# Performance work log

Measured on AMD Instinct MI355X. Metric: run time of the kernel, lower is better.

The kernel has to match this reference:

```python
import jax, jax.numpy as jnp
import numpy as np
import math

B, T, D, H = 4, 2048, 1024, 16
HD = D // H  # 64

def setup_inputs() -> dict:
    key = jax.random.key(0)
    ks = jax.random.split(key, 11)
    s = 1.0 / math.sqrt(D)
    return {
        "q": jax.random.normal(ks[0], (B, T, D), jnp.float32),
        "k": jax.random.normal(ks[1], (B, T, D), jnp.float32),
        "v": jax.random.normal(ks[2], (B, T, D), jnp.float32),
        "Wq": jax.random.normal(ks[3], (D, D), jnp.float32) * s,
        "bq": jnp.zeros((D,), jnp.float32),
        "Wk": jax.random.normal(ks[4], (D, D), jnp.float32) * s,
        "bk": jnp.zeros((D,), jnp.float32),
        "Wv": jax.random.normal(ks[5], (D, D), jnp.float32) * s,
        "bv": jnp.zeros((D,), jnp.float32),
        "Wo": jax.random.normal(ks[6], (D, D), jnp.float32) * s,
        "bo": jnp.zeros((D,), jnp.float32),
    }

def reference(q, k, v, Wq, bq, Wk, bk, Wv, bv, Wo, bo):
    # Linear projections (torch Linear: x @ W.T + b)
    qp = q @ Wq.T + bq
    kp = k @ Wk.T + bk
    vp = v @ Wv.T + bv
    # [B, T, D] -> [B, H, T, HD]
    def split(x):
        return x.reshape(B, T, H, HD).transpose(0, 2, 1, 3)
    qh, kh, vh = split(qp), split(kp), split(vp)
    # scaled dot-product attention
    score = jnp.einsum('bhqd,bhkd->bhqk', qh, kh) / math.sqrt(HD)
    attn = jax.nn.softmax(score, axis=-1)
    out = jnp.einsum('bhqk,bhkd->bhqd', attn, vh)
    # merge heads and output projection
    out = out.transpose(0, 2, 1, 3).reshape(B, T, D)
    return out @ Wo.T + bo
```

## Files before the change

kernel.cpp:

```cpp
#include <hip/hip_runtime.h>
#include <hip/hip_bf16.h>
#include <stdint.h>

#define B_ 4
#define T_ 2048
#define D_ 1024
#define H_ 16
#define HD_ 64
#define NKT (T_ / 64)

typedef __bf16 bf16;
typedef __bf16 bf16x8 __attribute__((ext_vector_type(8)));
typedef __bf16 bf16x4 __attribute__((ext_vector_type(4)));
typedef float f32x4 __attribute__((ext_vector_type(4)));
typedef uint32_t u32x4 __attribute__((ext_vector_type(4)));

#define QSCALE 0.18033688011112042f

__device__ __forceinline__ float fast_exp2(float x) {
#if __has_builtin(__builtin_amdgcn_exp2f)
    return __builtin_amdgcn_exp2f(x);
#else
    return exp2f(x);
#endif
}

__device__ __forceinline__ void async_load16(const bf16* g, const bf16* lds_uniform) {
    __builtin_amdgcn_global_load_lds(
        (const __attribute__((address_space(1))) uint32_t*)(uintptr_t)g,
        (__attribute__((address_space(3))) uint32_t*)(uintptr_t)lds_uniform,
        16, 0, 0);
}

__device__ __forceinline__ uint32_t pack2_bf16(float lo, float hi) {
    union { uint32_t u; __bf16 h[2]; } r;
    r.h[0] = (__bf16)lo;
    r.h[1] = (__bf16)hi;
    return r.u;
}

__device__ __forceinline__ void permswap16(uint32_t& a, uint32_t& b) {
    asm("v_permlane16_swap_b32 %0, %1" : "+v"(a), "+v"(b));
}

__global__ __launch_bounds__(256) void cast3(const float* __restrict__ s0, bf16* __restrict__ d0,
                                             const float* __restrict__ s1, bf16* __restrict__ d1,
                                             const float* __restrict__ s2, bf16* __restrict__ d2,
                                             int n4) {
    const float* s = blockIdx.y == 0 ? s0 : (blockIdx.y == 1 ? s1 : s2);
    bf16* d = blockIdx.y == 0 ? d0 : (blockIdx.y == 1 ? d1 : d2);
    int i = blockIdx.x * 256 + threadIdx.x;
    if (i < n4) {
        f32x4 v = ((const f32x4*)s)[i];
        bf16x4 o;
        o.x = (bf16)v.x; o.y = (bf16)v.y; o.z = (bf16)v.z; o.w = (bf16)v.w;
        ((bf16x4*)d)[i] = o;
    }
}

__global__ __launch_bounds__(256) void cast4(const float* __restrict__ s0, bf16* __restrict__ d0,
                                             const float* __restrict__ s1, bf16* __restrict__ d1,
                                             const float* __restrict__ s2, bf16* __restrict__ d2,
                                             const float* __restrict__ s3, bf16* __restrict__ d3,
                                             int n4) {
    const float* s = blockIdx.y == 0 ? s0 : (blockIdx.y == 1 ? s1 : (blockIdx.y == 2 ? s2 : s3));
    bf16* d = blockIdx.y == 0 ? d0 : (blockIdx.y == 1 ? d1 : (blockIdx.y == 2 ? d2 : d3));
    int i = blockIdx.x * 256 + threadIdx.x;
    if (i < n4) {
        f32x4 v = ((const f32x4*)s)[i];
        bf16x4 o;
        o.x = (bf16)v.x; o.y = (bf16)v.y; o.z = (bf16)v.z; o.w = (bf16)v.w;
        ((bf16x4*)d)[i] = o;
    }
}

template <typename OutT, int VMODE>
__device__ __forceinline__ void gemm_body(const bf16* __restrict__ A,
                                          const bf16* __restrict__ W,
                                          const float* __restrict__ bias,
                                          OutT* __restrict__ C,
                                          int lin, float scale,
                                          bf16* As, bf16* Bs, bf16* Tt) {
    const int K = D_, N = D_;
    const int tid = threadIdx.x;
    const int wid = tid >> 6, lane = tid & 63;
    const int quad = lane >> 4, l15 = lane & 15;
    const int wm = (wid >> 1) * 64, wn = (wid & 1) * 64;
    const int bx = N >> 7;
    const int ty = (lin & 7) + 8 * (lin / (8 * bx));
    const int tx = (lin >> 3) % bx;
    const long rowA0 = (long)ty * 128;
    const long rowB0 = (long)tx * 128;
    const int srow = lane >> 2;
    const int schunk = (lane & 3) * 8;
    const int sbase = (wid * 32) * 32;

    f32x4 acc[4][4];
#pragma unroll
    for (int i = 0; i < 4; i++)
#pragma unroll
        for (int j = 0; j < 4; j++) acc[i][j] = (f32x4){0.f, 0.f, 0.f, 0.f};

#pragma unroll
    for (int s = 0; s < 2; s++) {
        int r = wid * 32 + s * 16 + srow;
        async_load16(&A[(rowA0 + r) * K + schunk], &As[sbase + s * 16 * 32]);
        async_load16(&W[(rowB0 + r) * K + schunk], &Bs[sbase + s * 16 * 32]);
    }
    __syncthreads();

    const int NIT = K >> 5;
    for (int it = 0; it < NIT; it++) {
        const int cur = it & 1;
        const int co = cur * (128 * 32);
        if (it + 1 < NIT) {
            const int k1 = (it + 1) << 5;
            const int no = (cur ^ 1) * (128 * 32);
#pragma unroll
            for (int s = 0; s < 2; s++) {
                int r = wid * 32 + s * 16 + srow;
                async_load16(&A[(rowA0 + r) * K + k1 + schunk], &As[no + sbase + s * 16 * 32]);
                async_load16(&W[(rowB0 + r) * K + k1 + schunk], &Bs[no + sbase + s * 16 * 32]);
            }
        }
        bf16x8 af[4], bfr[4];
#pragma unroll
        for (int i = 0; i < 4; i++)
            af[i] = *(const bf16x8*)&As[co + (wm + i * 16 + l15) * 32 + quad * 8];
#pragma unroll
        for (int j = 0; j < 4; j++)
            bfr[j] = *(const bf16x8*)&Bs[co + (wn + j * 16 + l15) * 32 + quad * 8];
#pragma unroll
        for (int i = 0; i < 4; i++)
#pragma unroll
            for (int j = 0; j < 4; j++)
                acc[i][j] = __builtin_amdgcn_mfma_f32_16x16x32_bf16(af[i], bfr[j],
                                                                    acc[i][j], 0, 0, 0);
        __syncthreads();
    }

    if constexpr (VMODE == 0) {
#pragma unroll
        for (int i = 0; i < 4; i++) {
            long m = rowA0 + wm + i * 16 + quad * 4;
#pragma unroll
            for (int j = 0; j < 4; j++) {
                long n = rowB0 + wn + j * 16 + l15;
                float bb = bias[n];
#pragma unroll
                for (int r = 0; r < 4; r++) {
                    float v = (acc[i][j][r] + bb) * scale;
                    C[(m + r) * N + n] = (OutT)v;
                }
            }
        }
    } else {
#pragma unroll
        for (int i = 0; i < 4; i++) {
            int ml = wm + i * 16 + quad * 4;
#pragma unroll
            for (int j = 0; j < 4; j++) {
                int nl = wn + j * 16 + l15;
                float bb = bias[rowB0 + nl];
                bf16x4 ov = {(bf16)(acc[i][j][0] + bb), (bf16)(acc[i][j][1] + bb),
                             (bf16)(acc[i][j][2] + bb), (bf16)(acc[i][j][3] + bb)};
                *(bf16x4*)&Tt[nl * 136 + ml] = ov;
            }
        }
        __syncthreads();
        const long bidx = rowA0 >> 11;
        const int t0 = (int)(rowA0 & 2047);
#pragma unroll
        for (int p = 0; p < 8; p++) {
            int nl = p * 16 + (tid >> 4);
            int c = tid & 15;
            bf16x8 val = *(const bf16x8*)&Tt[nl * 136 + c * 8];
            int n = (int)rowB0 + nl;
            long vrow = (bidx * H_ + (n >> 6)) * (long)HD_ + (n & 63);
            int cp = (c & ~3) | ((c & 1) << 1) | ((c & 2) >> 1);
            *(bf16x8*)&((bf16*)C)[vrow * T_ + t0 + cp * 8] = val;
        }
    }
}

__global__ __launch_bounds__(256) void gemm_qkv(const bf16* __restrict__ Xq,
                                                const bf16* __restrict__ WqB,
                                                const float* __restrict__ bq,
                                                bf16* __restrict__ Qp,
                                                const bf16* __restrict__ Xk,
                                                const bf16* __restrict__ WkB,
                                                const float* __restrict__ bk,
                                                bf16* __restrict__ Kp,
                                                const bf16* __restrict__ Xv,
                                                const bf16* __restrict__ WvB,
                                                const float* __restrict__ bv,
                                                bf16* __restrict__ VtG) {
    __shared__ __align__(16) char sm[34816];
    bf16* As = (bf16*)sm;
    bf16* Bs = (bf16*)(sm + 16384);
    bf16* Tt = (bf16*)sm;
    const int p = blockIdx.x >> 9;
    const int lin = blockIdx.x & 511;
    if (p == 0)
        gemm_body<bf16, 0>(Xq, WqB, bq, Qp, lin, QSCALE, As, Bs, Tt);
    else if (p == 1)
        gemm_body<bf16, 0>(Xk, WkB, bk, Kp, lin, 1.f, As, Bs, Tt);
    else
        gemm_body<bf16, 1>(Xv, WvB, bv, VtG, lin, 1.f, As, Bs, Tt);
}

__global__ __launch_bounds__(256) void gemm_out(const bf16* __restrict__ Op,
                                                const bf16* __restrict__ WoB,
                                                const float* __restrict__ bo,
                                                float* __restrict__ out) {
    __shared__ __align__(16) char sm[32768];
    bf16* As = (bf16*)sm;
    bf16* Bs = (bf16*)(sm + 16384);
    gemm_body<float, 0>(Op, WoB, bo, out, blockIdx.x, 1.f, As, Bs, nullptr);
}

__global__ __launch_bounds__(256, 4) void attn_kernel(const bf16* __restrict__ Qp,
                                                      const bf16* __restrict__ Kp,
                                                      const bf16* __restrict__ VT,
                                                      bf16* __restrict__ Op) {
    __shared__ bf16 smem[4][64 * 64];
    const int tid = threadIdx.x;
    const int wid = tid >> 6, lane = tid & 63;
    const int quad = lane >> 4, l15 = lane & 15;
    const int q7 = l15 & 7;
    const int lin = blockIdx.x;
    const int bh = (lin & 7) + 8 * (lin >> 7);
    const int qt = (lin >> 3) & 15;
    const int b = bh >> 4, h = bh & 15;
    const long tok0 = (long)b * T_ + (long)qt * 128 + wid * 32;
    const int hcol = h * HD_;
    const long vrow0 = ((long)bh) * HD_;
    const int g_sw = ((lane & 7) ^ (lane >> 3)) * 8;
    const int srow = lane >> 3;
    const int sbase = (wid * 16) * 64;

    {
        const long krow0 = (long)b * T_;
#pragma unroll
        for (int s = 0; s < 2; s++) {
            int r = wid * 16 + s * 8 + srow;
            async_load16(&Kp[(krow0 + r) * D_ + hcol + g_sw], &smem[0][sbase + s * 8 * 64]);
            async_load16(&VT[(vrow0 + r) * T_ + g_sw], &smem[2][sbase + s * 8 * 64]);
        }
    }

    bf16x8 bq[2][2];
#pragma unroll
    for (int nt = 0; nt < 2; nt++)
#pragma unroll
        for (int ks = 0; ks < 2; ks++)
            bq[nt][ks] = *(const bf16x8*)&Qp[(tok0 + nt * 16 + l15) * D_ + hcol +
                                             ks * 32 + quad * 8];

    f32x4 o[4][2];
#pragma unroll
    for (int mt = 0; mt < 4; mt++)
#pragma unroll
        for (int nt = 0; nt < 2; nt++) o[mt][nt] = (f32x4){0.f, 0.f, 0.f, 0.f};
    float lsum[2] = {0.f, 0.f};

    __syncthreads();

    for (int kt = 0; kt < NKT; kt++) {
        const int cur = kt & 1;
        if (kt + 1 < NKT) {
            const long krow1 = (long)b * T_ + (long)(kt + 1) * 64;
            const int nb = cur ^ 1;
#pragma unroll
            for (int s = 0; s < 2; s++) {
                int r = wid * 16 + s * 8 + srow;
                async_load16(&Kp[(krow1 + r) * D_ + hcol + g_sw], &smem[nb][sbase + s * 8 * 64]);
                async_load16(&VT[(vrow0 + r) * T_ + (long)(kt + 1) * 64 + g_sw],
                             &smem[2 + nb][sbase + s * 8 * 64]);
            }
        }
        const bf16* Ksc = smem[cur];
        const bf16* Vsc = smem[2 + cur];

        bf16x8 pb0[2];
        {
            uint32_t pA[2][2], pB[2][2];
#pragma unroll
            for (int mt = 0; mt < 2; mt++) {
                bf16x8 ak0 = *(const bf16x8*)&Ksc[(mt * 16 + l15) * 64 + ((quad ^ q7) * 8)];
                bf16x8 ak1 = *(const bf16x8*)&Ksc[(mt * 16 + l15) * 64 + (((4 + quad) ^ q7) * 8)];
#pragma unroll
                for (int nt = 0; nt < 2; nt++) {
                    f32x4 s = {0.f, 0.f, 0.f, 0.f};
                    s = __builtin_amdgcn_mfma_f32_16x16x32_bf16(ak0, bq[nt][0], s, 0, 0, 0);
                    s = __builtin_amdgcn_mfma_f32_16x16x32_bf16(ak1, bq[nt][1], s, 0, 0, 0);
                    float p0 = fast_exp2(s[0]), p1 = fast_exp2(s[1]);
                    float p2 = fast_exp2(s[2]), p3 = fast_exp2(s[3]);
                    lsum[nt] += (p0 + p1) + (p2 + p3);
                    pA[mt][nt] = pack2_bf16(p0, p1);
                    pB[mt][nt] = pack2_bf16(p2, p3);
                }
            }
#pragma unroll
            for (int nt = 0; nt < 2; nt++) {
                permswap16(pA[0][nt], pA[1][nt]);
                permswap16(pB[0][nt], pB[1][nt]);
                u32x4 f = {pA[0][nt], pB[0][nt], pA[1][nt], pB[1][nt]};
                pb0[nt] = __builtin_bit_cast(bf16x8, f);
            }
        }
#pragma unroll
        for (int mt = 0; mt < 4; mt++) {
            bf16x8 av0 = *(const bf16x8*)&Vsc[(mt * 16 + l15) * 64 + ((quad ^ q7) * 8)];
#pragma unroll
            for (int nt = 0; nt < 2; nt++)
                o[mt][nt] = __builtin_amdgcn_mfma_f32_16x16x32_bf16(av0, pb0[nt],
                                                                    o[mt][nt], 0, 0, 0);
        }
        bf16x8 pb1[2];
        {
            uint32_t pA[2][2], pB[2][2];
#pragma unroll
            for (int mt = 0; mt < 2; mt++) {
                bf16x8 ak0 = *(const bf16x8*)&Ksc[((2 + mt) * 16 + l15) * 64 + ((quad ^ q7) * 8)];
                bf16x8 ak1 = *(const bf16x8*)&Ksc[((2 + mt) * 16 + l15) * 64 +
                                                  (((4 + quad) ^ q7) * 8)];
#pragma unroll
                for (int nt = 0; nt < 2; nt++) {
                    f32x4 s = {0.f, 0.f, 0.f, 0.f};
                    s = __builtin_amdgcn_mfma_f32_16x16x32_bf16(ak0, bq[nt][0], s, 0, 0, 0);
                    s = __builtin_amdgcn_mfma_f32_16x16x32_bf16(ak1, bq[nt][1], s, 0, 0, 0);
                    float p0 = fast_exp2(s[0]), p1 = fast_exp2(s[1]);
                    float p2 = fast_exp2(s[2]), p3 = fast_exp2(s[3]);
                    lsum[nt] += (p0 + p1) + (p2 + p3);
                    pA[mt][nt] = pack2_bf16(p0, p1);
                    pB[mt][nt] = pack2_bf16(p2, p3);
                }
            }
#pragma unroll
            for (int nt = 0; nt < 2; nt++) {
                permswap16(pA[0][nt], pA[1][nt]);
                permswap16(pB[0][nt], pB[1][nt]);
                u32x4 f = {pA[0][nt], pB[0][nt], pA[1][nt], pB[1][nt]};
                pb1[nt] = __builtin_bit_cast(bf16x8, f);
            }
        }
#pragma unroll
        for (int mt = 0; mt < 4; mt++) {
            bf16x8 av1 = *(const bf16x8*)&Vsc[(mt * 16 + l15) * 64 + (((4 + quad) ^ q7) * 8)];
#pragma unroll
            for (int nt = 0; nt < 2; nt++)
                o[mt][nt] = __builtin_amdgcn_mfma_f32_16x16x32_bf16(av1, pb1[nt],
                                                                    o[mt][nt], 0, 0, 0);
        }
        __syncthreads();
    }

#pragma unroll
    for (int nt = 0; nt < 2; nt++) {
        lsum[nt] += __shfl_xor(lsum[nt], 16, 64);
        lsum[nt] += __shfl_xor(lsum[nt], 32, 64);
        lsum[nt] = 1.f / lsum[nt];
    }

    bf16* ew = &smem[wid][0];
#pragma unroll
    for (int mt = 0; mt < 4; mt++)
#pragma unroll
        for (int nt = 0; nt < 2; nt++) {
            bf16x4 ov = {(bf16)(o[mt][nt][0] * lsum[nt]), (bf16)(o[mt][nt][1] * lsum[nt]),
                         (bf16)(o[mt][nt][2] * lsum[nt]), (bf16)(o[mt][nt][3] * lsum[nt])};
            *(bf16x4*)&ew[(nt * 16 + l15) * 64 +
                          (((mt * 2 + (quad >> 1)) ^ q7) * 8) + (quad & 1) * 4] = ov;
        }
#pragma unroll
    for (int p2 = 0; p2 < 4; p2++) {
        int q = p2 * 8 + (lane >> 3);
        int dc = lane & 7;
        bf16x8 ov = *(const bf16x8*)&ew[q * 64 + ((dc ^ (q & 7)) * 8)];
        *(bf16x8*)&Op[(tok0 + q) * D_ + hcol + dc * 8] = ov;
    }
}

extern "C" void kernel_launch(void* const* d_in, const int* in_sizes, int n_in,
                              void* d_out, int out_size, void* d_ws, size_t ws_size,
                              hipStream_t stream) {
    const float* q  = (const float*)d_in[0];
    const float* k  = (const float*)d_in[1];
    const float* v  = (const float*)d_in[2];
    const float* Wq = (const float*)d_in[3];
    const float* bq = (const float*)d_in[4];
    const float* Wk = (const float*)d_in[5];
    const float* bk = (const float*)d_in[6];
    const float* Wv = (const float*)d_in[7];
    const float* bv = (const float*)d_in[8];
    const float* Wo = (const float*)d_in[9];
    const float* bo = (const float*)d_in[10];
    float* out = (float*)d_out;

    const size_t MD = (size_t)B_ * T_ * D_;
    const size_t DD = (size_t)D_ * D_;
    char* ws = (char*)d_ws;
    bf16* Xq  = (bf16*)ws; ws += MD * 2;
    bf16* Xk  = (bf16*)ws; ws += MD * 2;
    bf16* Xv  = (bf16*)ws; ws += MD * 2;
    bf16* WqB = (bf16*)ws; ws += DD * 2;
    bf16* WkB = (bf16*)ws; ws += DD * 2;
    bf16* WvB = (bf16*)ws; ws += DD * 2;
    bf16* WoB = (bf16*)ws; ws += DD * 2;
    bf16* Qp  = (bf16*)ws; ws += MD * 2;
    bf16* Kp  = (bf16*)ws; ws += MD * 2;
    bf16* VtG = (bf16*)ws; ws += MD * 2;
    bf16* Op  = (bf16*)ws; ws += MD * 2;

    cast3<<<dim3(MD / 4 / 256, 3), 256, 0, stream>>>(q, Xq, k, Xk, v, Xv, MD / 4);
    cast4<<<dim3(DD / 4 / 256, 4), 256, 0, stream>>>(Wq, WqB, Wk, WkB, Wv, WvB, Wo, WoB, DD / 4);

    gemm_qkv<<<3 * 512, 256, 0, stream>>>(Xq, WqB, bq, Qp, Xk, WkB, bk, Kp, Xv, WvB, bv, VtG);

    attn_kernel<<<B_ * H_ * (T_ / 128), 256, 0, stream>>>(Qp, Kp, VtG, Op);

    gemm_out<<<512, 256, 0, stream>>>(Op, WoB, bo, out);
}
```

Measured before the change: 331.8 us.

## Use 8 waves per attention block with 16 query rows each, MFMA row sums

The attention kernel moves from 4 waves handling 32 query rows each to 8 waves handling 16 query rows each. Each wave now loads one row per K/V tile. This cuts per-wave register use and raises wave count for latency hiding. The softmax denominator is now computed with an MFMA against a ones vector instead of scalar adds and shuffles, and s_setprio brackets the PV MFMAs. In exchange, each K/V tile in shared memory is reused by fewer query rows per wave, and the MFMA count per block rises because of the extra row-sum MFMAs.

Measured after the change: 339.1 us. +2.2%, slower.

```diff
diff --git a/kernel.cpp b/kernel.cpp
--- a/kernel.cpp
+++ b/kernel.cpp
@@ -219,7 +219,7 @@
     gemm_body<float, 0>(Op, WoB, bo, out, blockIdx.x, 1.f, As, Bs, nullptr);
 }
 
-__global__ __launch_bounds__(256, 4) void attn_kernel(const bf16* __restrict__ Qp,
+__global__ __launch_bounds__(512, 8) void attn_kernel(const bf16* __restrict__ Qp,
                                                       const bf16* __restrict__ Kp,
                                                       const bf16* __restrict__ VT,
                                                       bf16* __restrict__ Op) {
@@ -232,37 +232,30 @@
     const int bh = (lin & 7) + 8 * (lin >> 7);
     const int qt = (lin >> 3) & 15;
     const int b = bh >> 4, h = bh & 15;
-    const long tok0 = (long)b * T_ + (long)qt * 128 + wid * 32;
+    const long tok0 = (long)b * T_ + (long)qt * 128 + wid * 16;
     const int hcol = h * HD_;
     const long vrow0 = ((long)bh) * HD_;
     const int g_sw = ((lane & 7) ^ (lane >> 3)) * 8;
     const int srow = lane >> 3;
-    const int sbase = (wid * 16) * 64;
+    const int sbase = (wid * 8) * 64;
 
     {
         const long krow0 = (long)b * T_;
-#pragma unroll
-        for (int s = 0; s < 2; s++) {
-            int r = wid * 16 + s * 8 + srow;
-            async_load16(&Kp[(krow0 + r) * D_ + hcol + g_sw], &smem[0][sbase + s * 8 * 64]);
-            async_load16(&VT[(vrow0 + r) * T_ + g_sw], &smem[2][sbase + s * 8 * 64]);
-        }
-    }
-
-    bf16x8 bq[2][2];
-#pragma unroll
-    for (int nt = 0; nt < 2; nt++)
-#pragma unroll
-        for (int ks = 0; ks < 2; ks++)
-            bq[nt][ks] = *(const bf16x8*)&Qp[(tok0 + nt * 16 + l15) * D_ + hcol +
-                                             ks * 32 + quad * 8];
-
-    f32x4 o[4][2];
-#pragma unroll
-    for (int mt = 0; mt < 4; mt++)
-#pragma unroll
-        for (int nt = 0; nt < 2; nt++) o[mt][nt] = (f32x4){0.f, 0.f, 0.f, 0.f};
-    float lsum[2] = {0.f, 0.f};
+        const int r = wid * 8 + srow;
+        async_load16(&Kp[(krow0 + r) * D_ + hcol + g_sw], &smem[0][sbase]);
+        async_load16(&VT[(vrow0 + r) * T_ + g_sw], &smem[2][sbase]);
+    }
+
+    bf16x8 bq0 = *(const bf16x8*)&Qp[(tok0 + l15) * D_ + hcol + quad * 8];
+    bf16x8 bq1 = *(const bf16x8*)&Qp[(tok0 + l15) * D_ + hcol + 32 + quad * 8];
+
+    const u32x4 onesu = {0x3F803F80u, 0x3F803F80u, 0x3F803F80u, 0x3F803F80u};
+    const bf16x8 ones = __builtin_bit_cast(bf16x8, onesu);
+
+    f32x4 o[4];
+#pragma unroll
+    for (int mt = 0; mt < 4; mt++) o[mt] = (f32x4){0.f, 0.f, 0.f, 0.f};
+    f32x4 ls = (f32x4){0.f, 0.f, 0.f, 0.f};
 
     __syncthreads();
 
@@ -271,110 +264,85 @@
         if (kt + 1 < NKT) {
             const long krow1 = (long)b * T_ + (long)(kt + 1) * 64;
             const int nb = cur ^ 1;
-#pragma unroll
-            for (int s = 0; s < 2; s++) {
-                int r = wid * 16 + s * 8 + srow;
-                async_load16(&Kp[(krow1 + r) * D_ + hcol + g_sw], &smem[nb][sbase + s * 8 * 64]);
-                async_load16(&VT[(vrow0 + r) * T_ + (long)(kt + 1) * 64 + g_sw],
-                             &smem[2 + nb][sbase + s * 8 * 64]);
-            }
+            const int r = wid * 8 + srow;
+            async_load16(&Kp[(krow1 + r) * D_ + hcol + g_sw], &smem[nb][sbase]);
+            async_load16(&VT[(vrow0 + r) * T_ + (long)(kt + 1) * 64 + g_sw],
+                         &smem[2 + nb][sbase]);
         }
         const bf16* Ksc = smem[cur];
         const bf16* Vsc = smem[2 + cur];
 
-        bf16x8 pb0[2];
+        bf16x8 pb0;
         {
-            uint32_t pA[2][2], pB[2][2];
+            uint32_t pA[2], pB[2];
 #pragma unroll
             for (int mt = 0; mt < 2; mt++) {
                 bf16x8 ak0 = *(const bf16x8*)&Ksc[(mt * 16 + l15) * 64 + ((quad ^ q7) * 8)];
                 bf16x8 ak1 = *(const bf16x8*)&Ksc[(mt * 16 + l15) * 64 + (((4 + quad) ^ q7) * 8)];
-#pragma unroll
-                for (int nt = 0; nt < 2; nt++) {
-                    f32x4 s = {0.f, 0.f, 0.f, 0.f};
-                    s = __builtin_amdgcn_mfma_f32_16x16x32_bf16(ak0, bq[nt][0], s, 0, 0, 0);
-                    s = __builtin_amdgcn_mfma_f32_16x16x32_bf16(ak1, bq[nt][1], s, 0, 0, 0);
-                    float p0 = fast_exp2(s[0]), p1 = fast_exp2(s[1]);
-                    float p2 = fast_exp2(s[2]), p3 = fast_exp2(s[3]);
-                    lsum[nt] += (p0 + p1) + (p2 + p3);
-                    pA[mt][nt] = pack2_bf16(p0, p1);
-                    pB[mt][nt] = pack2_bf16(p2, p3);
-                }
-            }
-#pragma unroll
-            for (int nt = 0; nt < 2; nt++) {
-                permswap16(pA[0][nt], pA[1][nt]);
-                permswap16(pB[0][nt], pB[1][nt]);
-                u32x4 f = {pA[0][nt], pB[0][nt], pA[1][nt], pB[1][nt]};
-                pb0[nt] = __builtin_bit_cast(bf16x8, f);
-            }
-        }
+                f32x4 s = {0.f, 0.f, 0.f, 0.f};
+                s = __builtin_amdgcn_mfma_f32_16x16x32_bf16(ak0, bq0, s, 0, 0, 0);
+                s = __builtin_amdgcn_mfma_f32_16x16x32_bf16(ak1, bq1, s, 0, 0, 0);
+                float p0 = fast_exp2(s[0]), p1 = fast_exp2(s[1]);
+                float p2 = fast_exp2(s[2]), p3 = fast_exp2(s[3]);
+                pA[mt] = pack2_bf16(p0, p1);
+                pB[mt] = pack2_bf16(p2, p3);
+            }
+            permswap16(pA[0], pA[1]);
+            permswap16(pB[0], pB[1]);
+            u32x4 f = {pA[0], pB[0], pA[1], pB[1]};
+            pb0 = __builtin_bit_cast(bf16x8, f);
+        }
+        __builtin_amdgcn_s_setprio(1);
+        ls = __builtin_amdgcn_mfma_f32_16x16x32_bf16(ones, pb0, ls, 0, 0, 0);
 #pragma unroll
         for (int mt = 0; mt < 4; mt++) {
             bf16x8 av0 = *(const bf16x8*)&Vsc[(mt * 16 + l15) * 64 + ((quad ^ q7) * 8)];
-#pragma unroll
-            for (int nt = 0; nt < 2; nt++)
-                o[mt][nt] = __builtin_amdgcn_mfma_f32_16x16x32_bf16(av0, pb0[nt],
-                                                                    o[mt][nt], 0, 0, 0);
-        }
-        bf16x8 pb1[2];
+            o[mt] = __builtin_amdgcn_mfma_f32_16x16x32_bf16(av0, pb0, o[mt], 0, 0, 0);
+        }
+        __builtin_amdgcn_s_setprio(0);
+        bf16x8 pb1;
         {
-            uint32_t pA[2][2], pB[2][2];
+            uint32_t pA[2], pB[2];
 #pragma unroll
             for (int mt = 0; mt < 2; mt++) {
                 bf16x8 ak0 = *(const bf16x8*)&Ksc[((2 + mt) * 16 + l15) * 64 + ((quad ^ q7) * 8)];
                 bf16x8 ak1 = *(const bf16x8*)&Ksc[((2 + mt) * 16 + l15) * 64 +
                                                   (((4 + quad) ^ q7) * 8)];
-#pragma unroll
-                for (int nt = 0; nt < 2; nt++) {
-                    f32x4 s = {0.f, 0.f, 0.f, 0.f};
-                    s = __builtin_amdgcn_mfma_f32_16x16x32_bf16(ak0, bq[nt][0], s, 0, 0, 0);
-                    s = __builtin_amdgcn_mfma_f32_16x16x32_bf16(ak1, bq[nt][1], s, 0, 0, 0);
-                    float p0 = fast_exp2(s[0]), p1 = fast_exp2(s[1]);
-                    float p2 = fast_exp2(s[2]), p3 = fast_exp2(s[3]);
-                    lsum[nt] += (p0 + p1) + (p2 + p3);
-                    pA[mt][nt] = pack2_bf16(p0, p1);
-                    pB[mt][nt] = pack2_bf16(p2, p3);
-                }
-            }
-#pragma unroll
-            for (int nt = 0; nt < 2; nt++) {
-                permswap16(pA[0][nt], pA[1][nt]);
-                permswap16(pB[0][nt], pB[1][nt]);
-                u32x4 f = {pA[0][nt], pB[0][nt], pA[1][nt], pB[1][nt]};
-                pb1[nt] = __builtin_bit_cast(bf16x8, f);
-            }
-        }
+                f32x4 s = {0.f, 0.f, 0.f, 0.f};
+                s = __builtin_amdgcn_mfma_f32_16x16x32_bf16(ak0, bq0, s, 0, 0, 0);
+                s = __builtin_amdgcn_mfma_f32_16x16x32_bf16(ak1, bq1, s, 0, 0, 0);
+                float p0 = fast_exp2(s[0]), p1 = fast_exp2(s[1]);
+                float p2 = fast_exp2(s[2]), p3 = fast_exp2(s[3]);
+                pA[mt] = pack2_bf16(p0, p1);
+                pB[mt] = pack2_bf16(p2, p3);
+            }
+            permswap16(pA[0], pA[1]);
+            permswap16(pB[0], pB[1]);
+            u32x4 f = {pA[0], pB[0], pA[1], pB[1]};
+            pb1 = __builtin_bit_cast(bf16x8, f);
+        }
+        __builtin_amdgcn_s_setprio(1);
+        ls = __builtin_amdgcn_mfma_f32_16x16x32_bf16(ones, pb1, ls, 0, 0, 0);
 #pragma unroll
         for (int mt = 0; mt < 4; mt++) {
             bf16x8 av1 = *(const bf16x8*)&Vsc[(mt * 16 + l15) * 64 + (((4 + quad) ^ q7) * 8)];
-#pragma unroll
-            for (int nt = 0; nt < 2; nt++)
-                o[mt][nt] = __builtin_amdgcn_mfma_f32_16x16x32_bf16(av1, pb1[nt],
-                                                                    o[mt][nt], 0, 0, 0);
-        }
+            o[mt] = __builtin_amdgcn_mfma_f32_16x16x32_bf16(av1, pb1, o[mt], 0, 0, 0);
+        }
+        __builtin_amdgcn_s_setprio(0);
         __syncthreads();
     }
 
-#pragma unroll
-    for (int nt = 0; nt < 2; nt++) {
-        lsum[nt] += __shfl_xor(lsum[nt], 16, 64);
-        lsum[nt] += __shfl_xor(lsum[nt], 32, 64);
-        lsum[nt] = 1.f / lsum[nt];
-    }
-
-    bf16* ew = &smem[wid][0];
-#pragma unroll
-    for (int mt = 0; mt < 4; mt++)
-#pragma unroll
-        for (int nt = 0; nt < 2; nt++) {
-            bf16x4 ov = {(bf16)(o[mt][nt][0] * lsum[nt]), (bf16)(o[mt][nt][1] * lsum[nt]),
-                         (bf16)(o[mt][nt][2] * lsum[nt]), (bf16)(o[mt][nt][3] * lsum[nt])};
-            *(bf16x4*)&ew[(nt * 16 + l15) * 64 +
-                          (((mt * 2 + (quad >> 1)) ^ q7) * 8) + (quad & 1) * 4] = ov;
-        }
-#pragma unroll
-    for (int p2 = 0; p2 < 4; p2++) {
+    const float linv = 1.f / ls[0];
+
+    bf16* ew = (bf16*)smem + wid * (16 * 64);
+#pragma unroll
+    for (int mt = 0; mt < 4; mt++) {
+        bf16x4 ov = {(bf16)(o[mt][0] * linv), (bf16)(o[mt][1] * linv),
+                     (bf16)(o[mt][2] * linv), (bf16)(o[mt][3] * linv)};
+        *(bf16x4*)&ew[l15 * 64 + (((mt * 2 + (quad >> 1)) ^ q7) * 8) + (quad & 1) * 4] = ov;
+    }
+#pragma unroll
+    for (int p2 = 0; p2 < 2; p2++) {
         int q = p2 * 8 + (lane >> 3);
         int dc = lane & 7;
         bf16x8 ov = *(const bf16x8*)&ew[q * 64 + ((dc ^ (q & 7)) * 8)];
@@ -418,7 +386,7 @@
 
     gemm_qkv<<<3 * 512, 256, 0, stream>>>(Xq, WqB, bq, Qp, Xk, WkB, bk, Kp, Xv, WvB, bv, VtG);
 
-    attn_kernel<<<B_ * H_ * (T_ / 128), 256, 0, stream>>>(Qp, Kp, VtG, Op);
+    attn_kernel<<<B_ * H_ * (T_ / 128), 512, 0, stream>>>(Qp, Kp, VtG, Op);
 
     gemm_out<<<512, 256, 0, stream>>>(Op, WoB, bo, out);
 }
```
